# Optimization experiments

Measured on AMD Instinct MI355X. Metric: run time of the kernel, lower is better.

## Reference

```python
import jax, jax.numpy as jnp
import numpy as np

B, S, N = 32, 64, 8192


def setup_inputs() -> dict:
    key = jax.random.key(0)
    k1, k2 = jax.random.split(key)
    x = jax.random.normal(k1, (B, S, N), dtype=jnp.float32)
    xref = jax.random.normal(k2, (B, S, N), dtype=jnp.float32)
    return {"x": x, "xref": xref}


def reference(x, xref):
    # Batched circular cross-correlation via FFT: corr = ifft(conj(fft(x)) * fft(xref)).real
    x32 = x.astype(jnp.float32)
    xref32 = xref.astype(jnp.float32)
    x_fft = jnp.fft.fft(x32, axis=-1)            # [B,S,N] complex64
    xref_fft = jnp.fft.fft(xref32, axis=-1)
    corr = jnp.real(jnp.fft.ifft(jnp.conj(x_fft) * xref_fft, axis=-1))  # [B,S,N]
    ind = jnp.argmax(corr, axis=-1)              # [B,S] int32
    n = x.shape[-1]
    # torch.roll(x, ind): out[k] = x[(k - ind) mod N]; vectorized circular shift via gather
    pos = (jnp.arange(n)[None, None, :] - ind[..., None]) % n  # [B,S,N]
    x_aligned = jnp.take_along_axis(x32, pos, axis=-1)
    inds = ind.astype(jnp.float32)               # original stores into a float zeros tensor
    return (x_aligned, inds)
```

## Files before the change

kernel.cpp:

```cpp
#include <hip/hip_runtime.h>
#include <hip/hip_bf16.h>

#define NFFT 8192
#define TPB  512
#define VPT  16

typedef float f2 __attribute__((ext_vector_type(2)));

__device__ __forceinline__ f2 mk(float a, float b){ f2 r; r.x=a; r.y=b; return r; }
__device__ __forceinline__ f2 cswap(f2 a){ return __builtin_shufflevector(a,a,1,0); }

__device__ __forceinline__ int swz(int j) { return j ^ ((j >> 4) & 15); }
__device__ __forceinline__ int rev13(unsigned x) { return (int)(__brev(x) >> 19); }

__device__ __forceinline__ f2 cmul_conj(f2 d, float c, float s){
  return d*c + cswap(d)*mk(s,-s);
}
__device__ __forceinline__ f2 cmul_pos(f2 v, float c, float s){
  return v*c + cswap(v)*mk(-s,s);
}

__device__ __forceinline__ void dif8_core(f2* y, int p_num, float inv_den) {
  float cA[4], sA[4], cB[2], sB[2], c4, s4;
  {
    float r = (float)p_num * inv_den;
    float sa = __builtin_amdgcn_sinf(r);
    float ca = __builtin_amdgcn_cosf(r);
    float c2 = ca*ca - sa*sa, s2 = 2.0f*ca*sa;
    c4 = c2*c2 - s2*s2; s4 = 2.0f*c2*s2;
    const float R = 0.70710678118654752f;
    cA[0] = ca;          sA[0] = sa;
    cA[1] = R*(ca-sa);   sA[1] = R*(ca+sa);
    cA[2] = -sa;         sA[2] = ca;
    cA[3] = -R*(ca+sa);  sA[3] = R*(ca-sa);
    cB[0] = c2;  sB[0] = s2;
    cB[1] = -s2; sB[1] = c2;
  }
  #pragma unroll
  for (int k = 0; k < 4; ++k) {
    f2 u = y[k], v = y[k+4];
    y[k] = u + v;
    y[k+4] = cmul_conj(u - v, cA[k], sA[k]);
  }
  #pragma unroll
  for (int h = 0; h < 8; h += 4)
    #pragma unroll
    for (int k0 = 0; k0 < 2; ++k0) {
      f2 u = y[h+k0], v = y[h+k0+2];
      y[h+k0] = u + v;
      y[h+k0+2] = cmul_conj(u - v, cB[k0], sB[k0]);
    }
  #pragma unroll
  for (int h = 0; h < 8; h += 2) {
    f2 u = y[h], v = y[h+1];
    y[h] = u + v;
    y[h+1] = cmul_conj(u - v, c4, s4);
  }
}

__device__ __forceinline__ void dit8_core(f2* y, int p_num, float inv_den) {
  float cA[4], sA[4], cB[2], sB[2], c4, s4;
  {
    float r = (float)p_num * inv_den;
    float sa = __builtin_amdgcn_sinf(r);
    float ca = __builtin_amdgcn_cosf(r);
    float c2 = ca*ca - sa*sa, s2 = 2.0f*ca*sa;
    c4 = c2*c2 - s2*s2; s4 = 2.0f*c2*s2;
    const float R = 0.70710678118654752f;
    cA[0] = ca;          sA[0] = sa;
    cA[1] = R*(ca-sa);   sA[1] = R*(ca+sa);
    cA[2] = -sa;         sA[2] = ca;
    cA[3] = -R*(ca+sa);  sA[3] = R*(ca-sa);
    cB[0] = c2;  sB[0] = s2;
    cB[1] = -s2; sB[1] = c2;
  }
  #pragma unroll
  for (int h = 0; h < 8; h += 2) {
    f2 u = y[h];
    f2 w = cmul_pos(y[h+1], c4, s4);
    y[h] = u + w; y[h+1] = u - w;
  }
  #pragma unroll
  for (int h = 0; h < 8; h += 4)
    #pragma unroll
    for (int k0 = 0; k0 < 2; ++k0) {
      f2 u = y[h+k0];
      f2 w = cmul_pos(y[h+k0+2], cB[k0], sB[k0]);
      y[h+k0] = u + w; y[h+k0+2] = u - w;
    }
  #pragma unroll
  for (int k = 0; k < 4; ++k) {
    f2 u = y[k];
    f2 w = cmul_pos(y[k+4], cA[k], sA[k]);
    y[k] = u + w; y[k+4] = u - w;
  }
}

__device__ __forceinline__ void dif_global1024(f2* z, int t) {
  #pragma unroll
  for (int gi = 0; gi < 2; ++gi) {
    int p = t + TPB*gi;
    f2* B = z + swz(p);
    f2 y[8];
    #pragma unroll
    for (int k = 0; k < 8; ++k) y[k] = B[1024*k];
    dif8_core(y, p, 0.125f/1024.0f);
    #pragma unroll
    for (int k = 0; k < 8; ++k) B[1024*k] = y[k];
  }
  __syncthreads();
}

__device__ __forceinline__ void dif_wave128(f2* z, int w, int l) {
  #pragma unroll
  for (int gi = 0; gi < 2; ++gi) {
    int gl = l + 64*gi;
    int E = swz(w*1024 + gl);
    f2* B0 = z + E;
    f2* B1 = z + (E ^ 8);
    f2 y[8];
    #pragma unroll
    for (int k = 0; k < 8; ++k) y[k] = (k&1) ? B1[128*k] : B0[128*k];
    dif8_core(y, gl, 0.125f/128.0f);
    #pragma unroll
    for (int k = 0; k < 8; ++k) { if (k&1) B1[128*k] = y[k]; else B0[128*k] = y[k]; }
  }
}

__device__ __forceinline__ void dit_wave128(f2* z, int w, int l) {
  #pragma unroll
  for (int gi = 0; gi < 2; ++gi) {
    int gl = l + 64*gi;
    int E = swz(w*1024 + gl);
    f2* B0 = z + E;
    f2* B1 = z + (E ^ 8);
    f2 y[8];
    #pragma unroll
    for (int k = 0; k < 8; ++k) y[k] = (k&1) ? B1[128*k] : B0[128*k];
    dit8_core(y, gl, 0.125f/128.0f);
    #pragma unroll
    for (int k = 0; k < 8; ++k) { if (k&1) B1[128*k] = y[k]; else B0[128*k] = y[k]; }
  }
}

__device__ __forceinline__ void dif_wave16(f2* z, int w, int l) {
  #pragma unroll
  for (int gi = 0; gi < 2; ++gi) {
    int gl = l + 64*gi;
    int p = gl & 15, blk = gl >> 4;
    int e = p ^ (8*(blk&1));
    f2* H = z + (w*1024 + blk*128);
    f2 y[8];
    #pragma unroll
    for (int k = 0; k < 8; ++k) y[k] = H[16*k + (e ^ k)];
    dif8_core(y, p, 0.125f/16.0f);
    #pragma unroll
    for (int k = 0; k < 8; ++k) H[16*k + (e ^ k)] = y[k];
  }
}

__device__ __forceinline__ void dit_wave16(f2* z, int w, int l) {
  #pragma unroll
  for (int gi = 0; gi < 2; ++gi) {
    int gl = l + 64*gi;
    int p = gl & 15, blk = gl >> 4;
    int e = p ^ (8*(blk&1));
    f2* H = z + (w*1024 + blk*128);
    f2 y[8];
    #pragma unroll
    for (int k = 0; k < 8; ++k) y[k] = H[16*k + (e ^ k)];
    dit8_core(y, p, 0.125f/16.0f);
    #pragma unroll
    for (int k = 0; k < 8; ++k) H[16*k + (e ^ k)] = y[k];
  }
}

#define C16_1 0.92387953251128674f
#define S16_1 0.38268343236508978f
#define RSQ2  0.70710678118654752f

__device__ __forceinline__ void dif16_x(f2* z, int t) {
  const float C8[8] = {1.f, C16_1, RSQ2, S16_1, 0.f, -S16_1, -RSQ2, -C16_1};
  const float S8[8] = {0.f, S16_1, RSQ2, C16_1, 1.f,  C16_1,  RSQ2,  S16_1};
  int e = t & 15;
  f2* H = z + 16*t;
  f2 y[16];
  #pragma unroll
  for (int c = 0; c < 16; ++c) y[c] = H[c ^ e];
  #pragma unroll
  for (int j = 0; j < 8; ++j) {
    f2 u = y[j], v = y[j+8];
    y[j] = u + v;
    y[j+8] = cmul_conj(u - v, C8[j], S8[j]);
  }
  #pragma unroll
  for (int h = 0; h < 16; h += 8)
    #pragma unroll
    for (int j = 0; j < 4; ++j) {
      f2 u = y[h+j], v = y[h+j+4];
      y[h+j] = u + v;
      y[h+j+4] = cmul_conj(u - v, C8[2*j], S8[2*j]);
    }
  #pragma unroll
  for (int h = 0; h < 16; h += 4)
    #pragma unroll
    for (int j = 0; j < 2; ++j) {
      f2 u = y[h+j], v = y[h+j+2];
      y[h+j] = u + v;
      f2 d = u - v;
      y[h+j+2] = j ? mk(d.y, -d.x) : d;
    }
  #pragma unroll
  for (int h = 0; h < 16; h += 2) {
    f2 u = y[h], v = y[h+1];
    y[h] = u + v; y[h+1] = u - v;
  }
  #pragma unroll
  for (int c = 0; c < 16; ++c) H[c ^ e] = y[c];
}

__device__ __forceinline__ void dit16_x(f2* z, int t) {
  const float C8[8] = {1.f, C16_1, RSQ2, S16_1, 0.f, -S16_1, -RSQ2, -C16_1};
  const float S8[8] = {0.f, S16_1, RSQ2, C16_1, 1.f,  C16_1,  RSQ2,  S16_1};
  int e = t & 15;
  f2* H = z + 16*t;
  f2 y[16];
  #pragma unroll
  for (int c = 0; c < 16; ++c) y[c] = H[c ^ e];
  #pragma unroll
  for (int h = 0; h < 16; h += 2) {
    f2 u = y[h], v = y[h+1];
    y[h] = u + v; y[h+1] = u - v;
  }
  #pragma unroll
  for (int h = 0; h < 16; h += 4)
    #pragma unroll
    for (int j = 0; j < 2; ++j) {
      f2 u = y[h+j];
      f2 v = y[h+j+2];
      f2 w = j ? mk(-v.y, v.x) : v;
      y[h+j] = u + w; y[h+j+2] = u - w;
    }
  #pragma unroll
  for (int h = 0; h < 16; h += 8)
    #pragma unroll
    for (int j = 0; j < 4; ++j) {
      f2 u = y[h+j];
      f2 w = cmul_pos(y[h+j+4], C8[2*j], S8[2*j]);
      y[h+j] = u + w; y[h+j+4] = u - w;
    }
  #pragma unroll
  for (int j = 0; j < 8; ++j) {
    f2 u = y[j];
    f2 w = cmul_pos(y[j+8], C8[j], S8[j]);
    y[j] = u + w; y[j+8] = u - w;
  }
  #pragma unroll
  for (int c = 0; c < 16; ++c) H[c ^ e] = y[c];
}

__device__ __forceinline__ void dit_last(const f2* z, int t, float* re, float& mv) {
  #pragma unroll
  for (int gi = 0; gi < 2; ++gi) {
    int g = t + TPB*gi;
    const f2* B = z + swz(g);
    f2 y[8];
    #pragma unroll
    for (int k = 0; k < 8; ++k) y[k] = B[1024*k];
    dit8_core(y, g, 0.125f/1024.0f);
    #pragma unroll
    for (int k = 0; k < 8; ++k) {
      re[8*gi + k] = y[k].x;
      mv = fmaxf(mv, y[k].x);
    }
  }
}

__global__ __launch_bounds__(TPB)
void corr_align_kernel(const float* __restrict__ x, const float* __restrict__ xref,
                       float* __restrict__ out0, float* __restrict__ outInd) {
  __shared__ f2 z[NFFT];
  const int t = threadIdx.x;
  const int lane = t & 63, wave = t >> 6;
  const int row = blockIdx.x;
  const float* xrow = x + (size_t)row * NFFT;
  const float* rrow = xref + (size_t)row * NFFT;

  const float4* x4 = (const float4*)xrow;
  const float4* r4 = (const float4*)rrow;
  #pragma unroll
  for (int gi = 0; gi < 4; ++gi) {
    int q = t + TPB*gi;
    float4 xv = x4[q], rv = r4[q];
    int j = 4*q;
    z[swz(j+0)] = mk(xv.x, rv.x);
    z[swz(j+1)] = mk(xv.y, rv.y);
    z[swz(j+2)] = mk(xv.z, rv.z);
    z[swz(j+3)] = mk(xv.w, rv.w);
  }
  __syncthreads();

  dif_global1024(z, t);
  dif_wave128(z, wave, lane);
  dif_wave16(z, wave, lane);
  dif16_x(z, t);
  __syncthreads();

  #pragma unroll
  for (int gi = 0; gi < 8; ++gi) {
    int k = 8*t + gi + 1;
    int p = rev13((unsigned)k);
    int q = rev13((unsigned)((NFFT - k) & (NFFT-1)));
    f2 Zp = z[swz(p)];
    f2 Zq = z[swz(q)];
    float Xx = 0.5f*(Zp.x + Zq.x);
    float Xy = 0.5f*(Zp.y - Zq.y);
    float Yx = 0.5f*(Zp.y + Zq.y);
    float Yy = 0.5f*(Zq.x - Zp.x);
    f2 Gk = mk(Xx*Yx + Xy*Yy, Xx*Yy - Xy*Yx);
    z[swz(p)] = Gk;
    if (k != NFFT/2) z[swz(q)] = mk(Gk.x, -Gk.y);
  }
  if (t == 0) {
    f2 Z0 = z[0];
    z[0] = mk(Z0.x * Z0.y, 0.0f);
  }
  __syncthreads();

  dit16_x(z, t);
  dit_wave16(z, wave, lane);
  dit_wave128(z, wave, lane);
  __syncthreads();
  float re[16];
  float mv = -3.0e38f;
  dit_last(z, t, re, mv);
  __syncthreads();

  float* zf = (float*)z;
  int*  zi = (int*)z;
  if (t == 0) zi[8] = 0;
  #pragma unroll
  for (int off = 32; off > 0; off >>= 1)
    mv = fmaxf(mv, __shfl_down(mv, off));
  if (lane == 0) zf[wave] = mv;
  __syncthreads();
  float M = zf[0];
  #pragma unroll
  for (int w = 1; w < 8; ++w) M = fmaxf(M, zf[w]);
  float thresh = M - 32768.0f;
  #pragma unroll
  for (int gi = 0; gi < 2; ++gi)
    #pragma unroll
    for (int k = 0; k < 8; ++k) {
      if (re[8*gi + k] >= thresh) {
        int pos = t + TPB*gi + 1024*k;
        int slot = atomicAdd(&zi[8], 1);
        if (slot < 40) zi[16 + slot] = pos;
      }
    }
  __syncthreads();
  int count = zi[8];
  if (count > 40) count = 40;

  int bestPos;
  if (count == 1) {
    bestPos = zi[16];
  } else {
    double* zd = (double*)z;
    double bestV = -1.0e300;
    int bp = NFFT;
    for (int c = 0; c < count; ++c) {
      int pos = zi[16 + c];
      double part = 0.0;
      #pragma unroll 4
      for (int gi = 0; gi < VPT; ++gi) {
        int n = t + TPB*gi;
        part += (double)xrow[n] * (double)rrow[(n + pos) & (NFFT-1)];
      }
      #pragma unroll
      for (int off = 32; off > 0; off >>= 1)
        part += __shfl_down(part, off);
      if (lane == 0) zd[32 + wave] = part;
      __syncthreads();
      if (t == 0) {
        double tot = 0.0;
        #pragma unroll
        for (int w = 0; w < 8; ++w) tot += zd[32 + w];
        if (tot > bestV || (tot == bestV && pos < bp)) { bestV = tot; bp = pos; }
      }
      __syncthreads();
    }
    if (t == 0) zi[9] = bp;
    __syncthreads();
    bestPos = zi[9];
  }

  float* orow = out0 + (size_t)row * NFFT;
  #pragma unroll 4
  for (int gi = 0; gi < VPT; ++gi) {
    int kk = t + TPB*gi;
    orow[kk] = xrow[(kk - bestPos) & (NFFT-1)];
  }
  if (t == 0) outInd[row] = (float)bestPos;
}

extern "C" void kernel_launch(void* const* d_in, const int* in_sizes, int n_in,
                              void* d_out, int out_size, void* d_ws, size_t ws_size,
                              hipStream_t stream) {
  const float* x    = (const float*)d_in[0];
  const float* xref = (const float*)d_in[1];
  float* out = (float*)d_out;
  const int rows = in_sizes[0] / NFFT;
  float* outInd = out + (size_t)rows * NFFT;
  hipLaunchKernelGGL(corr_align_kernel, dim3(rows), dim3(TPB), 0, stream,
                     x, xref, out, outInd);
}
```

Before: 230.1 us.

## Process multiple rows per block with register prefetch of next row

```diff
diff --git a/kernel.cpp b/kernel.cpp
--- a/kernel.cpp
+++ b/kernel.cpp
@@ -4,11 +4,16 @@
 #define NFFT 8192
 #define TPB  512
 #define VPT  16
+#define ROWS 4
 
 typedef float f2 __attribute__((ext_vector_type(2)));
 
 __device__ __forceinline__ f2 mk(float a, float b){ f2 r; r.x=a; r.y=b; return r; }
 __device__ __forceinline__ f2 cswap(f2 a){ return __builtin_shufflevector(a,a,1,0); }
+
+__device__ __forceinline__ void bar_lds() {
+  asm volatile("s_waitcnt lgkmcnt(0)\n\ts_barrier" ::: "memory");
+}
 
 __device__ __forceinline__ int swz(int j) { return j ^ ((j >> 4) & 15); }
 __device__ __forceinline__ int rev13(unsigned x) { return (int)(__brev(x) >> 19); }
@@ -108,7 +113,7 @@
     #pragma unroll
     for (int k = 0; k < 8; ++k) B[1024*k] = y[k];
   }
-  __syncthreads();
+  bar_lds();
 }
 
 __device__ __forceinline__ void dif_wave128(f2* z, int w, int l) {
@@ -276,132 +281,153 @@
   }
 }
 
-__global__ __launch_bounds__(TPB)
+__global__ __launch_bounds__(TPB, 4)
 void corr_align_kernel(const float* __restrict__ x, const float* __restrict__ xref,
-                       float* __restrict__ out0, float* __restrict__ outInd) {
+                       float* __restrict__ out0, float* __restrict__ outInd,
+                       int nrows) {
   __shared__ f2 z[NFFT];
   const int t = threadIdx.x;
   const int lane = t & 63, wave = t >> 6;
-  const int row = blockIdx.x;
-  const float* xrow = x + (size_t)row * NFFT;
-  const float* rrow = xref + (size_t)row * NFFT;
-
-  const float4* x4 = (const float4*)xrow;
-  const float4* r4 = (const float4*)rrow;
-  #pragma unroll
-  for (int gi = 0; gi < 4; ++gi) {
-    int q = t + TPB*gi;
-    float4 xv = x4[q], rv = r4[q];
-    int j = 4*q;
-    z[swz(j+0)] = mk(xv.x, rv.x);
-    z[swz(j+1)] = mk(xv.y, rv.y);
-    z[swz(j+2)] = mk(xv.z, rv.z);
-    z[swz(j+3)] = mk(xv.w, rv.w);
-  }
-  __syncthreads();
-
-  dif_global1024(z, t);
-  dif_wave128(z, wave, lane);
-  dif_wave16(z, wave, lane);
-  dif16_x(z, t);
-  __syncthreads();
-
-  #pragma unroll
-  for (int gi = 0; gi < 8; ++gi) {
-    int k = 8*t + gi + 1;
-    int p = rev13((unsigned)k);
-    int q = rev13((unsigned)((NFFT - k) & (NFFT-1)));
-    f2 Zp = z[swz(p)];
-    f2 Zq = z[swz(q)];
-    float Xx = 0.5f*(Zp.x + Zq.x);
-    float Xy = 0.5f*(Zp.y - Zq.y);
-    float Yx = 0.5f*(Zp.y + Zq.y);
-    float Yy = 0.5f*(Zq.x - Zp.x);
-    f2 Gk = mk(Xx*Yx + Xy*Yy, Xx*Yy - Xy*Yx);
-    z[swz(p)] = Gk;
-    if (k != NFFT/2) z[swz(q)] = mk(Gk.x, -Gk.y);
-  }
-  if (t == 0) {
-    f2 Z0 = z[0];
-    z[0] = mk(Z0.x * Z0.y, 0.0f);
-  }
-  __syncthreads();
-
-  dit16_x(z, t);
-  dit_wave16(z, wave, lane);
-  dit_wave128(z, wave, lane);
-  __syncthreads();
-  float re[16];
-  float mv = -3.0e38f;
-  dit_last(z, t, re, mv);
-  __syncthreads();
-
-  float* zf = (float*)z;
-  int*  zi = (int*)z;
-  if (t == 0) zi[8] = 0;
-  #pragma unroll
-  for (int off = 32; off > 0; off >>= 1)
-    mv = fmaxf(mv, __shfl_down(mv, off));
-  if (lane == 0) zf[wave] = mv;
-  __syncthreads();
-  float M = zf[0];
-  #pragma unroll
-  for (int w = 1; w < 8; ++w) M = fmaxf(M, zf[w]);
-  float thresh = M - 32768.0f;
-  #pragma unroll
-  for (int gi = 0; gi < 2; ++gi)
-    #pragma unroll
-    for (int k = 0; k < 8; ++k) {
-      if (re[8*gi + k] >= thresh) {
-        int pos = t + TPB*gi + 1024*k;
-        int slot = atomicAdd(&zi[8], 1);
-        if (slot < 40) zi[16 + slot] = pos;
+  const int row0 = blockIdx.x * ROWS;
+  const int rmax = (nrows - row0 < ROWS) ? (nrows - row0) : ROWS;
+
+  float4 sx[4], sr[4];
+  {
+    const float4* x4 = (const float4*)(x + (size_t)row0 * NFFT);
+    const float4* r4 = (const float4*)(xref + (size_t)row0 * NFFT);
+    #pragma unroll
+    for (int gi = 0; gi < 4; ++gi) { int q = t + TPB*gi; sx[gi] = x4[q]; sr[gi] = r4[q]; }
+  }
+
+  for (int r = 0; r < rmax; ++r) {
+    const int row = row0 + r;
+    const float* xrow = x + (size_t)row * NFFT;
+    const float* rrow = xref + (size_t)row * NFFT;
+
+    bar_lds();
+
+    #pragma unroll
+    for (int gi = 0; gi < 4; ++gi) {
+      int q = t + TPB*gi;
+      float4 xv = sx[gi], rv = sr[gi];
+      int j = 4*q;
+      z[swz(j+0)] = mk(xv.x, rv.x);
+      z[swz(j+1)] = mk(xv.y, rv.y);
+      z[swz(j+2)] = mk(xv.z, rv.z);
+      z[swz(j+3)] = mk(xv.w, rv.w);
+    }
+    bar_lds();
+
+    if (r + 1 < rmax) {
+      const float4* x4 = (const float4*)(x + (size_t)(row + 1) * NFFT);
+      const float4* r4 = (const float4*)(xref + (size_t)(row + 1) * NFFT);
+      #pragma unroll
+      for (int gi = 0; gi < 4; ++gi) { int q = t + TPB*gi; sx[gi] = x4[q]; sr[gi] = r4[q]; }
+    }
+
+    dif_global1024(z, t);
+    dif_wave128(z, wave, lane);
+    dif_wave16(z, wave, lane);
+    dif16_x(z, t);
+    bar_lds();
+
+    #pragma unroll
+    for (int gi = 0; gi < 8; ++gi) {
+      int k = 8*t + gi + 1;
+      int p = rev13((unsigned)k);
+      int q = rev13((unsigned)((NFFT - k) & (NFFT-1)));
+      f2 Zp = z[swz(p)];
+      f2 Zq = z[swz(q)];
+      float Xx = 0.5f*(Zp.x + Zq.x);
+      float Xy = 0.5f*(Zp.y - Zq.y);
+      float Yx = 0.5f*(Zp.y + Zq.y);
+      float Yy = 0.5f*(Zq.x - Zp.x);
+      f2 Gk = mk(Xx*Yx + Xy*Yy, Xx*Yy - Xy*Yx);
+      z[swz(p)] = Gk;
+      if (k != NFFT/2) z[swz(q)] = mk(Gk.x, -Gk.y);
+    }
+    if (t == 0) {
+      f2 Z0 = z[0];
+      z[0] = mk(Z0.x * Z0.y, 0.0f);
+    }
+    bar_lds();
+
+    dit16_x(z, t);
+    dit_wave16(z, wave, lane);
+    dit_wave128(z, wave, lane);
+    bar_lds();
+    float re[16];
+    float mv = -3.0e38f;
+    dit_last(z, t, re, mv);
+    bar_lds();
+
+    float* zf = (float*)z;
+    int*  zi = (int*)z;
+    if (t == 0) zi[8] = 0;
+    #pragma unroll
+    for (int off = 32; off > 0; off >>= 1)
+      mv = fmaxf(mv, __shfl_down(mv, off));
+    if (lane == 0) zf[wave] = mv;
+    bar_lds();
+    float M = zf[0];
+    #pragma unroll
+    for (int w = 1; w < 8; ++w) M = fmaxf(M, zf[w]);
+    float thresh = M - 32768.0f;
+    #pragma unroll
+    for (int gi = 0; gi < 2; ++gi)
+      #pragma unroll
+      for (int k = 0; k < 8; ++k) {
+        if (re[8*gi + k] >= thresh) {
+          int pos = t + TPB*gi + 1024*k;
+          int slot = atomicAdd(&zi[8], 1);
+          if (slot < 40) zi[16 + slot] = pos;
+        }
       }
-    }
-  __syncthreads();
-  int count = zi[8];
-  if (count > 40) count = 40;
-
-  int bestPos;
-  if (count == 1) {
-    bestPos = zi[16];
-  } else {
-    double* zd = (double*)z;
-    double bestV = -1.0e300;
-    int bp = NFFT;
-    for (int c = 0; c < count; ++c) {
-      int pos = zi[16 + c];
-      double part = 0.0;
-      #pragma unroll 4
-      for (int gi = 0; gi < VPT; ++gi) {
-        int n = t + TPB*gi;
-        part += (double)xrow[n] * (double)rrow[(n + pos) & (NFFT-1)];
+    bar_lds();
+    int count = zi[8];
+    if (count > 40) count = 40;
+
+    int bestPos;
+    if (count == 1) {
+      bestPos = zi[16];
+    } else {
+      double* zd = (double*)z;
+      double bestV = -1.0e300;
+      int bp = NFFT;
+      for (int c = 0; c < count; ++c) {
+        int pos = zi[16 + c];
+        double part = 0.0;
+        #pragma unroll 4
+        for (int gi = 0; gi < VPT; ++gi) {
+          int n = t + TPB*gi;
+          part += (double)xrow[n] * (double)rrow[(n + pos) & (NFFT-1)];
+        }
+        #pragma unroll
+        for (int off = 32; off > 0; off >>= 1)
+          part += __shfl_down(part, off);
+        if (lane == 0) zd[32 + wave] = part;
+        bar_lds();
+        if (t == 0) {
+          double tot = 0.0;
+          #pragma unroll
+          for (int w = 0; w < 8; ++w) tot += zd[32 + w];
+          if (tot > bestV || (tot == bestV && pos < bp)) { bestV = tot; bp = pos; }
+        }
+        bar_lds();
       }
-      #pragma unroll
-      for (int off = 32; off > 0; off >>= 1)
-        part += __shfl_down(part, off);
-      if (lane == 0) zd[32 + wave] = part;
-      __syncthreads();
-      if (t == 0) {
-        double tot = 0.0;
-        #pragma unroll
-        for (int w = 0; w < 8; ++w) tot += zd[32 + w];
-        if (tot > bestV || (tot == bestV && pos < bp)) { bestV = tot; bp = pos; }
-      }
-      __syncthreads();
-    }
-    if (t == 0) zi[9] = bp;
-    __syncthreads();
-    bestPos = zi[9];
-  }
-
-  float* orow = out0 + (size_t)row * NFFT;
-  #pragma unroll 4
-  for (int gi = 0; gi < VPT; ++gi) {
-    int kk = t + TPB*gi;
-    orow[kk] = xrow[(kk - bestPos) & (NFFT-1)];
-  }
-  if (t == 0) outInd[row] = (float)bestPos;
+      if (t == 0) zi[9] = bp;
+      bar_lds();
+      bestPos = zi[9];
+    }
+
+    float* orow = out0 + (size_t)row * NFFT;
+    #pragma unroll 4
+    for (int gi = 0; gi < VPT; ++gi) {
+      int kk = t + TPB*gi;
+      orow[kk] = xrow[(kk - bestPos) & (NFFT-1)];
+    }
+    if (t == 0) outInd[row] = (float)bestPos;
+  }
 }
 
 extern "C" void kernel_launch(void* const* d_in, const int* in_sizes, int n_in,
@@ -412,6 +438,7 @@
   float* out = (float*)d_out;
   const int rows = in_sizes[0] / NFFT;
   float* outInd = out + (size_t)rows * NFFT;
-  hipLaunchKernelGGL(corr_align_kernel, dim3(rows), dim3(TPB), 0, stream,
-                     x, xref, out, outInd);
-}
+  const int grid = (rows + ROWS - 1) / ROWS;
+  hipLaunchKernelGGL(corr_align_kernel, dim3(grid), dim3(TPB), 0, stream,
+                     x, xref, out, outInd, rows);
+}
```

After: 565.8 us. 146% more time.
